# Performance work log

Measured on AMD Instinct MI355X. Metric: run time of the kernel, lower is better.

## Reference

```python
import jax, jax.numpy as jnp
import numpy as np

EPS = 0.1
MAX_ITER = 100
THRESH = 0.1


def setup_inputs() -> dict:
    key = jax.random.key(0)
    k1, k2 = jax.random.split(key)
    N = 4096
    x = jax.random.normal(k1, (N, N), dtype=jnp.float32)
    y = jax.random.normal(k2, (N, N), dtype=jnp.float32)
    return {"x": x, "y": y}


def _sinkhorn(x, y):
    # forward softmaxes inputs along last dim
    x = jax.nn.softmax(x, axis=-1)
    y = jax.nn.softmax(y, axis=-1)
    # squared-euclidean cost |x_i - y_j|^2, expanded to avoid an [N,N,D] broadcast
    x2 = jnp.sum(x * x, axis=-1)  # [n]
    y2 = jnp.sum(y * y, axis=-1)  # [m]
    C = x2[:, None] + y2[None, :] - 2.0 * (x @ y.T)  # [n, m]
    n = x.shape[-1]  # source sizes mu/nu by the FEATURE dim (requires n == m == d)
    log_mu = jnp.log(jnp.full((n,), 1.0 / n, dtype=C.dtype) + 1e-8)
    log_nu = log_mu

    def M(u, v):
        # faithful to source: both u and v broadcast over the COLUMN axis
        return (-C + u[None, :] + v[None, :]) / EPS

    def step(carry, _):
        u, v, done = carry
        u1 = u
        u_new = EPS * (log_mu - jax.nn.logsumexp(M(u, v), axis=-1)) + u
        v_new = EPS * (log_nu - jax.nn.logsumexp(M(u_new, v).T, axis=-1)) + v
        # torch: (u-u1).abs().sum(-1).mean() with implicit batch of 1 == plain sum
        err = jnp.sum(jnp.abs(u_new - u1))
        u = jnp.where(done, u, u_new)
        v = jnp.where(done, v, v_new)
        return (u, v, done | (err < THRESH)), None

    init = (jnp.zeros((n,), C.dtype), jnp.zeros((n,), C.dtype), jnp.array(False))
    (u, v, _), _ = jax.lax.scan(step, init, None, length=MAX_ITER)
    pi = jnp.exp(M(u, v))  # [n, m] (torch returns [1, n, m]; batch dim squeezed)
    cost = jnp.sum(pi * C)  # cost.mean() over the singleton batch == scalar sum
    return cost, pi, C


def reference(x, y):
    return _sinkhorn(x, y)
```

## Files before the change

kernel.cpp:

```cpp
#include <hip/hip_runtime.h>
#include <math.h>

#define NN 4096

typedef __bf16 bf16;
typedef __attribute__((ext_vector_type(4))) __bf16 bf16x4;
typedef __attribute__((ext_vector_type(8))) __bf16 bf16x8;
typedef __attribute__((ext_vector_type(4))) float f32x4;

__device__ __forceinline__ void gld16(const void* g, void* l) {
  __builtin_amdgcn_global_load_lds((const __attribute__((address_space(1))) void*)g,
                                   (__attribute__((address_space(3))) void*)l, 16, 0, 0);
}


__device__ __forceinline__ double blockSumD(double v) {
  __shared__ double w[4];
  #pragma unroll
  for (int o = 32; o > 0; o >>= 1) v += __shfl_down(v, o, 64);
  __syncthreads();
  if ((threadIdx.x & 63) == 0) w[threadIdx.x >> 6] = v;
  __syncthreads();
  return w[0] + w[1] + w[2] + w[3];
}

__device__ __forceinline__ float blockMaxF(float v) {
  __shared__ float w[4];
  #pragma unroll
  for (int o = 32; o > 0; o >>= 1) v = fmaxf(v, __shfl_down(v, o, 64));
  __syncthreads();
  if ((threadIdx.x & 63) == 0) w[threadIdx.x >> 6] = v;
  __syncthreads();
  return fmaxf(fmaxf(w[0], w[1]), fmaxf(w[2], w[3]));
}


__global__ void softmax_rows(const float* __restrict__ x, const float* __restrict__ y,
                             bf16* __restrict__ xh, bf16* __restrict__ yh,
                             float* __restrict__ rowsq, float* __restrict__ out) {
  int row = blockIdx.x;
  int t = threadIdx.x;
  if (row == 0 && t == 0) out[0] = 0.0f;
  int r = (row < NN) ? row : row - NN;
  const f32x4* __restrict__ src = (const f32x4*)(((row < NN) ? x : y) + (size_t)r * NN);
  bf16x4* __restrict__ dst = (bf16x4*)(((row < NN) ? xh : yh) + (size_t)r * NN);

  f32x4 v[4];
  float m = -3.402823466e38f;
  #pragma unroll
  for (int j = 0; j < 4; ++j) {
    v[j] = src[t + 256 * j];
    m = fmaxf(fmaxf(fmaxf(m, v[j].x), fmaxf(v[j].y, v[j].z)), v[j].w);
  }
  float M = blockMaxF(m);

  float s = 0.0f;
  #pragma unroll
  for (int j = 0; j < 4; ++j) {
    v[j].x = __expf(v[j].x - M); v[j].y = __expf(v[j].y - M);
    v[j].z = __expf(v[j].z - M); v[j].w = __expf(v[j].w - M);
    s += (v[j].x + v[j].y) + (v[j].z + v[j].w);
  }
  double S = blockSumD((double)s);
  float inv = (float)(1.0 / S);

  float q = 0.0f;
  #pragma unroll
  for (int j = 0; j < 4; ++j) {
    f32x4 p = v[j] * inv;
    bf16x4 h;
    h.x = (bf16)p.x; h.y = (bf16)p.y; h.z = (bf16)p.z; h.w = (bf16)p.w;
    dst[t + 256 * j] = h;
    q += (p.x * p.x + p.y * p.y) + (p.z * p.z + p.w * p.w);
  }
  double Q = blockSumD((double)q);
  if (t == 0) rowsq[row] = (float)Q;
}


__global__ __launch_bounds__(256) void gemm_bt(const bf16* __restrict__ A,
                                               const bf16* __restrict__ B,
                                               const float* __restrict__ rowsq,
                                               float* __restrict__ C,
                                               float* __restrict__ colpart) {
  __shared__ __align__(16) bf16 As[128 * 64];
  __shared__ __align__(16) bf16 Bs[128 * 64];
  __shared__ float lsc[2][128];
  int t = threadIdx.x;
  int i0 = blockIdx.y * 128;
  int j0 = blockIdx.x * 128;
  int w = t >> 6, l = t & 63;
  int mrow = (w >> 1) * 64, ncol = (w & 1) * 64;
  int lr = l & 15, lq = l >> 4;

  f32x4 acc[4][4] = {};

  for (int kc = 0; kc < NN; kc += 64) {
    __syncthreads();
    #pragma unroll
    for (int q = 0; q < 4; ++q) {
      int c = t + 256 * q;
      int row = c >> 3;
      int jg = (c & 7) ^ (row & 7);
      gld16(A + (size_t)(i0 + row) * NN + kc + jg * 8, (char*)As + c * 16);
    }
    #pragma unroll
    for (int q = 0; q < 4; ++q) {
      int c = t + 256 * q;
      int row = c >> 3;
      int jg = (c & 7) ^ (row & 7);
      gld16(B + (size_t)(j0 + row) * NN + kc + jg * 8, (char*)Bs + c * 16);
    }
    __syncthreads();

    #pragma unroll
    for (int s = 0; s < 2; ++s) {
      bf16x8 af[4], bg[4];
      #pragma unroll
      for (int i = 0; i < 4; ++i) {
        int ra = mrow + 16 * i + lr;
        int ja = (s * 4 + lq) ^ (ra & 7);
        af[i] = *(const bf16x8*)((const char*)As + (ra * 8 + ja) * 16);
        int rb = ncol + 16 * i + lr;
        int jb = (s * 4 + lq) ^ (rb & 7);
        bg[i] = *(const bf16x8*)((const char*)Bs + (rb * 8 + jb) * 16);
      }
      #pragma unroll
      for (int i = 0; i < 4; ++i)
        #pragma unroll
        for (int jj = 0; jj < 4; ++jj)
          acc[i][jj] = __builtin_amdgcn_mfma_f32_16x16x32_bf16(af[i], bg[jj], acc[i][jj], 0, 0, 0);
    }
  }

  float y2v[4], ec[4] = {0.f, 0.f, 0.f, 0.f};
  #pragma unroll
  for (int jj = 0; jj < 4; ++jj) y2v[jj] = rowsq[NN + j0 + ncol + 16 * jj + lr];
  #pragma unroll
  for (int i = 0; i < 4; ++i) {
    #pragma unroll
    for (int r = 0; r < 4; ++r) {
      int grow = i0 + mrow + 16 * i + lq * 4 + r;
      float x2 = rowsq[grow];
      size_t rowoff = (size_t)grow * NN + j0 + ncol;
      #pragma unroll
      for (int jj = 0; jj < 4; ++jj) {
        float cv = x2 + y2v[jj] - 2.0f * acc[i][jj][r];
        C[rowoff + 16 * jj + lr] = cv;
        ec[jj] += __expf(-10.0f * cv);
      }
    }
  }
  #pragma unroll
  for (int jj = 0; jj < 4; ++jj) {
    ec[jj] += __shfl_xor(ec[jj], 16, 64);
    ec[jj] += __shfl_xor(ec[jj], 32, 64);
  }
  if (lq == 0) {
    #pragma unroll
    for (int jj = 0; jj < 4; ++jj) lsc[w >> 1][ncol + 16 * jj + lr] = ec[jj];
  }
  __syncthreads();
  if (t < 128) colpart[(size_t)blockIdx.y * NN + j0 + t] = lsc[0][t] + lsc[1][t];
}


__global__ void pi_cost_fused(const float* __restrict__ Cm, const float* __restrict__ colpart,
                              float* __restrict__ pi, float* __restrict__ out) {
  __shared__ float sdl[128];
  int t = threadIdx.x;
  int j0 = blockIdx.x * 128;
  int r0 = blockIdx.y * 128;
  if (t < 128) {
    double s = 0.0;
    #pragma unroll
    for (int ch = 0; ch < 32; ++ch) s += (double)colpart[(size_t)ch * NN + j0 + t];
    sdl[t] = (float)(-8.317725207557924 - log(s));
  }
  __syncthreads();

  int col = t & 127, rh = t >> 7;
  float sj = sdl[col];
  float facc = 0.0f;
  #pragma unroll 8
  for (int rr = 0; rr < 64; ++rr) {
    int row = r0 + rr * 2 + rh;
    size_t idx = (size_t)row * NN + j0 + col;
    float c = Cm[idx];
    float p = __expf(fmaf(-10.0f, c, sj));
    pi[idx] = p;
    facc = fmaf(p, c, facc);
  }
  double total = blockSumD((double)facc);
  if (t == 0) atomicAdd(out, (float)total);
}


extern "C" void kernel_launch(void* const* d_in, const int* in_sizes, int n_in,
                              void* d_out, int out_size, void* d_ws, size_t ws_size,
                              hipStream_t stream) {
  const float* x = (const float*)d_in[0];
  const float* y = (const float*)d_in[1];
  float* out = (float*)d_out;
  float* pi = out + 1;
  float* Cm = out + 1 + (size_t)NN * NN;

  char* ws = (char*)d_ws;
  bf16* xh = (bf16*)ws;
  bf16* yh = xh + (size_t)NN * NN;
  size_t off = (size_t)NN * NN * 2 * 2;
  float* rowsq = (float*)(ws + off);       off += 2 * NN * 4;
  float* colpart = (float*)(ws + off);     off += 32 * NN * 4;

  hipLaunchKernelGGL(softmax_rows, dim3(2 * NN), dim3(256), 0, stream, x, y, xh, yh, rowsq, out);
  hipLaunchKernelGGL(gemm_bt, dim3(32, 32), dim3(256), 0, stream, xh, yh, rowsq, Cm, colpart);
  hipLaunchKernelGGL(pi_cost_fused, dim3(32, 32), dim3(256), 0, stream, Cm, colpart, pi, out);
}
```

Baseline: 403.6 us.

## Vectorize pi/cost pass with aligned 16-byte accesses and split column LSE kernel

The pi/cost kernel now processes C and pi as 16-byte vectors. Since pi starts at out+1, the vectors are offset by 3 floats so that pi+3 is 16-byte aligned. The few leftover elements at each end are handled by one thread. Column log-sum-exp finalisation moves into a separate small kernel writing a padded vector, so it is no longer recomputed by every block. Softmax writes bf16 in 8-wide contiguous chunks per thread. This adds a fourth kernel launch and more complex indexing.

Result: no change. 410.3 us (+1.6%).

```diff
diff --git a/kernel.cpp b/kernel.cpp
--- a/kernel.cpp
+++ b/kernel.cpp
@@ -4,7 +4,6 @@
 #define NN 4096
 
 typedef __bf16 bf16;
-typedef __attribute__((ext_vector_type(4))) __bf16 bf16x4;
 typedef __attribute__((ext_vector_type(8))) __bf16 bf16x8;
 typedef __attribute__((ext_vector_type(4))) float f32x4;
 
@@ -43,13 +42,13 @@
   if (row == 0 && t == 0) out[0] = 0.0f;
   int r = (row < NN) ? row : row - NN;
   const f32x4* __restrict__ src = (const f32x4*)(((row < NN) ? x : y) + (size_t)r * NN);
-  bf16x4* __restrict__ dst = (bf16x4*)(((row < NN) ? xh : yh) + (size_t)r * NN);
+  bf16x8* __restrict__ dst = (bf16x8*)(((row < NN) ? xh : yh) + (size_t)r * NN);
 
   f32x4 v[4];
   float m = -3.402823466e38f;
   #pragma unroll
   for (int j = 0; j < 4; ++j) {
-    v[j] = src[t + 256 * j];
+    v[j] = src[4 * t + j];
     m = fmaxf(fmaxf(fmaxf(m, v[j].x), fmaxf(v[j].y, v[j].z)), v[j].w);
   }
   float M = blockMaxF(m);
@@ -66,12 +65,15 @@
 
   float q = 0.0f;
   #pragma unroll
-  for (int j = 0; j < 4; ++j) {
-    f32x4 p = v[j] * inv;
-    bf16x4 h;
-    h.x = (bf16)p.x; h.y = (bf16)p.y; h.z = (bf16)p.z; h.w = (bf16)p.w;
-    dst[t + 256 * j] = h;
-    q += (p.x * p.x + p.y * p.y) + (p.z * p.z + p.w * p.w);
+  for (int j = 0; j < 2; ++j) {
+    f32x4 p0 = v[2 * j] * inv;
+    f32x4 p1 = v[2 * j + 1] * inv;
+    bf16x8 h;
+    h[0] = (bf16)p0.x; h[1] = (bf16)p0.y; h[2] = (bf16)p0.z; h[3] = (bf16)p0.w;
+    h[4] = (bf16)p1.x; h[5] = (bf16)p1.y; h[6] = (bf16)p1.z; h[7] = (bf16)p1.w;
+    dst[2 * t + j] = h;
+    q += (p0.x * p0.x + p0.y * p0.y) + (p0.z * p0.z + p0.w * p0.w);
+    q += (p1.x * p1.x + p1.y * p1.y) + (p1.z * p1.z + p1.w * p1.w);
   }
   double Q = blockSumD((double)q);
   if (t == 0) rowsq[row] = (float)Q;
@@ -165,31 +167,54 @@
 }
 
 
-__global__ void pi_cost_fused(const float* __restrict__ Cm, const float* __restrict__ colpart,
-                              float* __restrict__ pi, float* __restrict__ out) {
-  __shared__ float sdl[128];
+__global__ void col_lse_final(const float* __restrict__ colpart, float* __restrict__ sdfp) {
+  int col = blockIdx.x * 256 + threadIdx.x;
+  double s = 0.0;
+  #pragma unroll
+  for (int ch = 0; ch < 32; ++ch) s += (double)colpart[(size_t)ch * NN + col];
+  float val = (float)(-8.317725207557924 - log(s));
+  sdfp[col] = val;
+  if (col < 4) sdfp[4096 + col] = val;
+}
+
+
+__global__ void pi_cost(const float* __restrict__ Cm, const float* __restrict__ sdfp,
+                        float* __restrict__ pi, float* __restrict__ out) {
   int t = threadIdx.x;
-  int j0 = blockIdx.x * 128;
-  int r0 = blockIdx.y * 128;
-  if (t < 128) {
-    double s = 0.0;
-    #pragma unroll
-    for (int ch = 0; ch < 32; ++ch) s += (double)colpart[(size_t)ch * NN + j0 + t];
-    sdl[t] = (float)(-8.317725207557924 - log(s));
-  }
-  __syncthreads();
-
-  int col = t & 127, rh = t >> 7;
-  float sj = sdl[col];
+  float sj[4][4];
+  #pragma unroll
+  for (int jm = 0; jm < 4; ++jm) {
+    int c0 = 3 + 4 * ((t + 256 * jm) & 1023);
+    sj[jm][0] = sdfp[c0];     sj[jm][1] = sdfp[c0 + 1];
+    sj[jm][2] = sdfp[c0 + 2]; sj[jm][3] = sdfp[c0 + 3];
+  }
+  size_t qbase = (size_t)blockIdx.x * 2048 + t;
   float facc = 0.0f;
-  #pragma unroll 8
-  for (int rr = 0; rr < 64; ++rr) {
-    int row = r0 + rr * 2 + rh;
-    size_t idx = (size_t)row * NN + j0 + col;
-    float c = Cm[idx];
-    float p = __expf(fmaf(-10.0f, c, sj));
-    pi[idx] = p;
-    facc = fmaf(p, c, facc);
+  #pragma unroll
+  for (int j = 0; j < 8; ++j) {
+    size_t q = qbase + 256 * j;
+    if (q < 4194303) {
+      const f32x4 c = *(const f32x4*)(Cm + 3 + 4 * q);
+      f32x4 p;
+      p.x = __expf(fmaf(-10.0f, c.x, sj[j & 3][0]));
+      p.y = __expf(fmaf(-10.0f, c.y, sj[j & 3][1]));
+      p.z = __expf(fmaf(-10.0f, c.z, sj[j & 3][2]));
+      p.w = __expf(fmaf(-10.0f, c.w, sj[j & 3][3]));
+      *(f32x4*)(pi + 3 + 4 * q) = p;
+      facc = fmaf(p.x, c.x, facc); facc = fmaf(p.y, c.y, facc);
+      facc = fmaf(p.z, c.z, facc); facc = fmaf(p.w, c.w, facc);
+    }
+  }
+  if (blockIdx.x == 0 && t == 0) {
+    const size_t es[4] = {0, 1, 2, (size_t)NN * NN - 1};
+    #pragma unroll
+    for (int k = 0; k < 4; ++k) {
+      size_t e = es[k];
+      float cv = Cm[e];
+      float p = __expf(fmaf(-10.0f, cv, sdfp[(int)(e & (NN - 1))]));
+      pi[e] = p;
+      facc = fmaf(p, cv, facc);
+    }
   }
   double total = blockSumD((double)facc);
   if (t == 0) atomicAdd(out, (float)total);
@@ -211,8 +236,10 @@
   size_t off = (size_t)NN * NN * 2 * 2;
   float* rowsq = (float*)(ws + off);       off += 2 * NN * 4;
   float* colpart = (float*)(ws + off);     off += 32 * NN * 4;
+  float* sdfp = (float*)(ws + off);        off += 4100 * 4;
 
   hipLaunchKernelGGL(softmax_rows, dim3(2 * NN), dim3(256), 0, stream, x, y, xh, yh, rowsq, out);
   hipLaunchKernelGGL(gemm_bt, dim3(32, 32), dim3(256), 0, stream, xh, yh, rowsq, Cm, colpart);
-  hipLaunchKernelGGL(pi_cost_fused, dim3(32, 32), dim3(256), 0, stream, Cm, colpart, pi, out);
-}
+  hipLaunchKernelGGL(col_lse_final, dim3(16), dim3(256), 0, stream, colpart, sdfp);
+  hipLaunchKernelGGL(pi_cost, dim3(2048), dim3(256), 0, stream, Cm, sdfp, pi, out);
+}
```
